# Kernel optimization log

Measured on AMD Instinct MI355X. Metric: run time of the kernel, lower is better.

The kernel has to match this reference:

```python
import jax, jax.numpy as jnp
import numpy as np

V = 32000   # vocab_size
S = 4096    # seq_len
D = 1024    # dim
H = 4096    # hidden_dim
L = 2       # num_layers
CS = 64     # chunk_size
R = 256     # low_rank_dim = max(8, D//4)
WIN = 8     # window_size (OptitationLayer default)
NEG = -1e30


def setup_inputs() -> dict:
    key = jax.random.key(0)
    ks = jax.random.split(key, 20)
    f32 = jnp.float32
    inp = {}
    inp['idx_seq'] = jax.random.randint(ks[0], (S,), 0, V)
    inp['embeddings'] = jax.random.normal(ks[1], (V, D), f32) * 0.01
    inp['positional'] = jax.random.normal(ks[2], (S, D), f32) * 0.01
    # per-layer MLP params, stacked over layer axis
    inp['Wg'] = jax.random.normal(ks[3], (L, D, D), f32) / D ** 0.5
    inp['bg'] = jnp.zeros((L, D), f32)
    inp['Ws'] = jax.random.normal(ks[4], (L, D, H), f32) / D ** 0.5
    inp['bs'] = jnp.zeros((L, H), f32)
    inp['Wo'] = jax.random.normal(ks[5], (L, H, D), f32) / H ** 0.5
    inp['bo'] = jnp.zeros((L, D), f32)
    # per-layer optitation (windowed attention) params
    inp['Wq'] = jax.random.normal(ks[6], (L, D, R), f32) / D ** 0.5
    inp['Wk'] = jax.random.normal(ks[7], (L, D, R), f32) / D ** 0.5
    inp['Wv'] = jax.random.normal(ks[8], (L, D, R), f32) / D ** 0.5
    inp['Wao'] = jax.random.normal(ks[9], (L, R, D), f32) / R ** 0.5
    inp['bq'] = jnp.zeros((L, R), f32)
    inp['bk'] = jnp.zeros((L, R), f32)
    inp['bv'] = jnp.zeros((L, R), f32)
    inp['bao'] = jnp.zeros((L, D), f32)
    inp['outW'] = jax.random.normal(ks[10], (D, V), f32) / D ** 0.5
    inp['outb'] = jnp.zeros((V,), f32)
    return inp


def _optitation(x, Wq, bq, Wk, bk, Wv, bv, Wao, bao):
    Q = x @ Wq + bq
    K = x @ Wk + bk
    Vv = x @ Wv + bv
    s = x.shape[0]
    off = jnp.arange(WIN + 1)
    j = jnp.arange(s)[:, None] - off[None, :]  # [s, w+1] key indices
    valid = j >= 0
    jc = jnp.maximum(j, 0)
    Kw = K[jc]   # [s, w+1, R]
    Vw = Vv[jc]  # [s, w+1, R]
    scores = jnp.einsum('sr,swr->sw', Q, Kw) / jnp.sqrt(jnp.float32(R))
    scores = jnp.where(valid, scores, NEG)
    attn = jax.nn.softmax(scores, axis=-1)
    ao = jnp.einsum('sw,swr->sr', attn, Vw)   # [s, R]
    return ao @ Wao + bao


def _chunk_link(x):
    # chunk-averaging with half-weighted neighbor chunks
    s, d = x.shape
    pad = (-s) % CS
    xp = jnp.pad(x, ((0, pad), (0, 0)))
    n = xp.shape[0] // CS
    c = xp.reshape(n, CS, d)
    prev = jnp.concatenate([jnp.zeros_like(c[:1]), c[:-1]], axis=0)
    nxt = jnp.concatenate([c[1:], jnp.zeros_like(c[:1])], axis=0)
    i = jnp.arange(n)
    w = 1.0 + 0.5 * (i > 0).astype(x.dtype) + 0.5 * (i < n - 1).astype(x.dtype)
    upd = (c + 0.5 * prev + 0.5 * nxt) / w[:, None, None]
    return upd.reshape(-1, d)[:s]


def reference(idx_seq, embeddings, positional, Wg, bg, Ws, bs, Wo, bo,
              Wq, bq, Wk, bk, Wv, bv, Wao, bao, outW, outb):
    s = idx_seq.shape[0]
    x = embeddings[idx_seq] + positional[:s]
    # decay accumulation: x[pos] += 0.8**pos * x[0] for pos >= 1 (x[0] untouched)
    decay = jnp.power(jnp.float32(0.8), jnp.arange(s, dtype=jnp.float32))
    decay = decay.at[0].set(0.0)
    x = x + decay[:, None] * x[0]
    for l in range(L):
        residual = x
        x = x * jax.nn.sigmoid(x @ Wg[l] + bg[l])            # lensed gate
        x = jnp.tanh(x @ Ws[l] + bs[l]) @ Wo[l] + bo[l]       # context sculpt
        x = x + residual
        x = x + _optitation(x, Wq[l], bq[l], Wk[l], bk[l],
                            Wv[l], bv[l], Wao[l], bao[l])
        x = _chunk_link(x)
    return x @ outW + outb
```

## Files before the change

kernel.cpp:

```cpp
#include <hip/hip_runtime.h>
#include <hip/hip_bf16.h>
#include <math.h>

#define S_LEN 4096
#define DIM   1024
#define HID   4096
#define NLAYER 2
#define RDIM  256
#define VOCAB 32000
#define QKVN  768

typedef unsigned short u16;
typedef __attribute__((ext_vector_type(8))) short s16x8;
typedef __attribute__((ext_vector_type(4))) float f32x4;
typedef __attribute__((ext_vector_type(4))) unsigned short u16x4;

__device__ inline u16 f2b(float f){
  unsigned u = __float_as_uint(f);
  u += 0x7fff + ((u >> 16) & 1);
  return (u16)(u >> 16);
}

__device__ inline void gload_lds16(const void* g, void* l){
  __builtin_amdgcn_global_load_lds((__attribute__((address_space(1))) void*)(g),
                                   (__attribute__((address_space(3))) void*)(l), 16, 0, 0);
}

__global__ void k_prep(const float* __restrict__ Wg,  const float* __restrict__ Ws,
                       const float* __restrict__ Wo,  const float* __restrict__ Wq,
                       const float* __restrict__ Wk,  const float* __restrict__ Wv,
                       const float* __restrict__ Wao, const float* __restrict__ outW,
                       u16* __restrict__ WgT, u16* __restrict__ WsT, u16* __restrict__ WoT,
                       u16* __restrict__ WqkvT, u16* __restrict__ WaoT, u16* __restrict__ outWT,
                       const float* __restrict__ bq, const float* __restrict__ bk,
                       const float* __restrict__ bv, float* __restrict__ bqkv2,
                       const int* __restrict__ idx, const float* __restrict__ emb,
                       const float* __restrict__ pos, float* __restrict__ xf,
                       u16* __restrict__ xb){
  __shared__ float tile[64][65];
  int tx = threadIdx.x, ty = threadIdx.y;
  int t = ty * 16 + tx;
  int id = blockIdx.x;
  if (id < 16384){
    int s = id >> 2;
    int d = (id & 3) * 256 + t;
    float v = emb[(size_t)idx[s] * DIM + d] + pos[(size_t)s * DIM + d];
    if (s > 0){
      float x0 = emb[(size_t)idx[0] * DIM + d] + pos[d];
      v += exp2f((float)s * -0.3219280948873623f) * x0;
    }
    size_t o = (size_t)s * DIM + d;
    xf[o] = v; xb[o] = f2b(v);
    return;
  }
  id -= 16384;
  if (id < 6){
    int l = id / 3, sel = id % 3;
    const float* s = sel == 0 ? bq : (sel == 1 ? bk : bv);
    bqkv2[l * 768 + sel * 256 + t] = s[(size_t)l * 256 + t];
    return;
  }
  id -= 6;
  const float* src; u16* dst; int K, N, bx, by;
  if (id < 512){
    int z = id >> 8, lo = id & 255;
    src = Wg + (size_t)z * DIM * DIM; dst = WgT + (size_t)z * DIM * DIM;
    K = DIM; N = DIM; bx = lo & 15; by = lo >> 4;
  } else if (id < 2560){
    int local = id - 512; int z = local >> 10, lo = local & 1023;
    src = Ws + (size_t)z * DIM * HID; dst = WsT + (size_t)z * DIM * HID;
    K = DIM; N = HID; bx = lo & 63; by = lo >> 6;
  } else if (id < 4608){
    int local = id - 2560; int z = local >> 10, lo = local & 1023;
    src = Wo + (size_t)z * HID * DIM; dst = WoT + (size_t)z * HID * DIM;
    K = HID; N = DIM; bx = lo & 15; by = lo >> 4;
  } else if (id < 4736){
    int local = id - 4608; int z = local >> 6, lo = local & 63;
    src = Wq + (size_t)z * DIM * RDIM; dst = WqkvT + (size_t)z * QKVN * DIM;
    K = DIM; N = RDIM; bx = lo & 3; by = lo >> 2;
  } else if (id < 4864){
    int local = id - 4736; int z = local >> 6, lo = local & 63;
    src = Wk + (size_t)z * DIM * RDIM; dst = WqkvT + (size_t)z * QKVN * DIM + (size_t)256 * DIM;
    K = DIM; N = RDIM; bx = lo & 3; by = lo >> 2;
  } else if (id < 4992){
    int local = id - 4864; int z = local >> 6, lo = local & 63;
    src = Wv + (size_t)z * DIM * RDIM; dst = WqkvT + (size_t)z * QKVN * DIM + (size_t)512 * DIM;
    K = DIM; N = RDIM; bx = lo & 3; by = lo >> 2;
  } else if (id < 5120){
    int local = id - 4992; int z = local >> 6, lo = local & 63;
    src = Wao + (size_t)z * RDIM * DIM; dst = WaoT + (size_t)z * RDIM * DIM;
    K = RDIM; N = DIM; bx = lo & 15; by = lo >> 4;
  } else {
    int local = id - 5120;
    src = outW; dst = outWT;
    K = DIM; N = VOCAB; bx = local % 500; by = local / 500;
  }
  int n0 = bx * 64, k0 = by * 64;
  #pragma unroll
  for (int i = 0; i < 4; i++){
    float4 v = *(const float4*)&src[(size_t)(k0 + ty + 16 * i) * N + n0 + tx * 4];
    tile[ty + 16 * i][tx * 4 + 0] = v.x;
    tile[ty + 16 * i][tx * 4 + 1] = v.y;
    tile[ty + 16 * i][tx * 4 + 2] = v.z;
    tile[ty + 16 * i][tx * 4 + 3] = v.w;
  }
  __syncthreads();
  #pragma unroll
  for (int i = 0; i < 4; i++){
    u16x4 o;
    #pragma unroll
    for (int j = 0; j < 4; j++) o[j] = f2b(tile[tx * 4 + j][ty + 16 * i]);
    *(u16x4*)&dst[(size_t)(n0 + ty + 16 * i) * K + k0 + tx * 4] = o;
  }
}

#define EP_GATE  0
#define EP_TANH  1
#define EP_RESID 2
#define EP_BIASF 3
#define EP_AO    4
#define EP_OUT   5

#define PH_SYNC() do{ asm volatile("" ::: "memory"); __builtin_amdgcn_s_barrier(); asm volatile("" ::: "memory"); }while(0)


#define MMA_QUAD(MH, NLO, BF) \
  { _Pragma("unroll") for (int mi = 0; mi < 4; mi++){ \
    _Pragma("unroll") for (int ni = 0; ni < 2; ni++){ \
      _Pragma("unroll") for (int ks = 0; ks < 2; ks++){ \
        acc[(MH)*4+mi][(NLO)+ni] = __builtin_amdgcn_mfma_f32_16x16x32_bf16((BF)[ni*2+ks], af[mi*2+ks], acc[(MH)*4+mi][(NLO)+ni], 0, 0, 0); } } } }

#define LDA(MH, BO) \
  { _Pragma("unroll") for (int mi = 0; mi < 4; mi++){ \
    _Pragma("unroll") for (int ks = 0; ks < 2; ks++){ \
      af[mi*2+ks] = *(const s16x8*)(pa0 + (BO) + ((MH)*4+mi)*1024 + ((ks ^ kb) * 32)); } } }

#define LDB(NH, BO) \
  { _Pragma("unroll") for (int ni = 0; ni < 2; ni++){ \
    _Pragma("unroll") for (int ks = 0; ks < 2; ks++){ \
      bf_[(NH)*4+ni*2+ks] = *(const s16x8*)(pb0 + (BO) + ((NH)*2+ni)*1024 + ((ks ^ kb) * 32)); } } }

__global__ __launch_bounds__(512, 2) void k_gemmL(
    const u16* __restrict__ A, const u16* __restrict__ Bt,
    const float* __restrict__ bias, float* __restrict__ outf,
    int N, int K, int tilesM, int tilesN){
  extern __shared__ u16 lds[];
  const int t = threadIdx.x;
  const int w = t >> 6, l = t & 63;
  const int wr = w >> 2, wc = w & 3;
  const int NT = K >> 6;
  const int NI = NT >> 1;
  const int nTiles = tilesM * tilesN;

  const int r0 = t >> 3;
  const int scol = (((t & 7) ^ ((t >> 3) & 7)) * 8);
  const int cb = (((l >> 4) ^ (l & 3)) * 8);
  const int kb = (l >> 2) & 1;
  const u16* pa0 = lds + (wr * 128 + (l & 15)) * 64 + cb;
  const u16* pb0 = lds + 32768 + (wc * 64 + (l & 15)) * 64 + cb;

  auto decode = [&](int idx2, int& bR, int& bC){
    int pr = tilesN * 2;
    int stripe = idx2 / pr, r2 = idx2 % pr;
    bR = (stripe * 2 + (r2 & 1)) * 256;
    bC = (r2 >> 1) * 256;
  };

  int tileIdx = blockIdx.x;
  if (tileIdx >= nTiles) return;
  int bRow, bCol, nRow = 0, nCol = 0;
  bool hasNext = false;
  decode(tileIdx, bRow, bCol);

  auto stage_half = [&](int tau, int q){
    const u16* base;
    if (tau >= NT){
      if (!hasNext) return;
      tau -= NT;
      base = (q < 2) ? A + (size_t)nRow * K : Bt + (size_t)nCol * K;
    } else {
      base = (q < 2) ? A + (size_t)bRow * K : Bt + (size_t)bCol * K;
    }
    int h = q & 1;
    const u16* gp = base + (size_t)(h * 128 + r0) * K + (size_t)tau * 64 + scol;
    u16* d = lds + ((q < 2) ? 0 : 32768) + ((tau & 1) * 16384) + h * 8192 + t * 8;
    gload_lds16(gp, d);
    gload_lds16(gp + (size_t)64 * K, d + 4096);
  };

  f32x4 acc[8][4] = {};
  s16x8 af[8], bf_[8];

  stage_half(0, 0); stage_half(0, 1); stage_half(0, 2); stage_half(0, 3);
  stage_half(1, 0);
  asm volatile("s_waitcnt vmcnt(2)" ::: "memory");
  PH_SYNC();

  for (; tileIdx < nTiles; tileIdx += gridDim.x){
    int nIdx = tileIdx + gridDim.x;
    hasNext = nIdx < nTiles;
    if (hasNext) decode(nIdx, nRow, nCol);

    for (int i = 0; i < NI; i++){
      const int t1 = 2 * i + 1, t2 = 2 * i + 2, t3 = 2 * i + 3;
      const bool lastGate = (!hasNext) && (i + 1 == NI);
      LDA(0, 0); LDB(0, 0);
      stage_half(t1, 1);
      PH_SYNC();
      __builtin_amdgcn_s_setprio(1); MMA_QUAD(0, 0, bf_); __builtin_amdgcn_s_setprio(0);
      PH_SYNC();
      LDB(1, 0);
      stage_half(t1, 2);
      PH_SYNC();
      __builtin_amdgcn_s_setprio(1); MMA_QUAD(0, 2, bf_ + 4); __builtin_amdgcn_s_setprio(0);
      PH_SYNC();
      LDA(1, 0);
      stage_half(t1, 3);
      PH_SYNC();
      __builtin_amdgcn_s_setprio(1); MMA_QUAD(1, 2, bf_ + 4); __builtin_amdgcn_s_setprio(0);
      PH_SYNC();
      stage_half(t2, 0);
      if (!lastGate) asm volatile("s_waitcnt vmcnt(2)" ::: "memory");
      else           asm volatile("s_waitcnt vmcnt(0)" ::: "memory");
      PH_SYNC();
      __builtin_amdgcn_s_setprio(1); MMA_QUAD(1, 0, bf_); __builtin_amdgcn_s_setprio(0);
      PH_SYNC();
      LDA(0, 16384); LDB(0, 16384);
      stage_half(t2, 1);
      PH_SYNC();
      __builtin_amdgcn_s_setprio(1); MMA_QUAD(0, 0, bf_); __builtin_amdgcn_s_setprio(0);
      PH_SYNC();
      LDB(1, 16384);
      stage_half(t2, 2);
      PH_SYNC();
      __builtin_amdgcn_s_setprio(1); MMA_QUAD(0, 2, bf_ + 4); __builtin_amdgcn_s_setprio(0);
      PH_SYNC();
      LDA(1, 16384);
      stage_half(t2, 3);
      PH_SYNC();
      __builtin_amdgcn_s_setprio(1); MMA_QUAD(1, 2, bf_ + 4); __builtin_amdgcn_s_setprio(0);
      PH_SYNC();
      stage_half(t3, 0);
      if (!lastGate) asm volatile("s_waitcnt vmcnt(2)" ::: "memory");
      PH_SYNC();
      __builtin_amdgcn_s_setprio(1); MMA_QUAD(1, 0, bf_); __builtin_amdgcn_s_setprio(0);
      PH_SYNC();
    }

    #pragma unroll
    for (int m = 0; m < 8; m++){
      int gr = bRow + wr * 128 + m * 16 + (l & 15);
      #pragma unroll
      for (int n = 0; n < 4; n++){
        int gc = bCol + wc * 64 + n * 16 + ((l >> 4) * 4);
        f32x4 v = acc[m][n] + *(const f32x4*)(bias + gc);
        *(f32x4*)(outf + (size_t)gr * N + gc) = v;
        acc[m][n] = (f32x4){0.f, 0.f, 0.f, 0.f};
      }
    }
    bRow = nRow; bCol = nCol;
  }
}

#define MMA2(MH, NL) \
  { _Pragma("unroll") for (int mi = 0; mi < 2; mi++){ \
    _Pragma("unroll") for (int ks = 0; ks < 2; ks++){ \
      acc[(MH)*2+mi][(NL)] = __builtin_amdgcn_mfma_f32_16x16x32_bf16(bf_[(NL)*2+ks], af[mi*2+ks], acc[(MH)*2+mi][(NL)], 0, 0, 0); } } }

#define LDA2(MH, BO) \
  { _Pragma("unroll") for (int mi = 0; mi < 2; mi++){ \
    _Pragma("unroll") for (int ks = 0; ks < 2; ks++){ \
      af[mi*2+ks] = *(const s16x8*)(pa0 + (BO) + ((MH)*2+mi)*1024 + ((ks ^ kb) * 32)); } } }

#define LDB2(NL, BO) \
  { _Pragma("unroll") for (int ks = 0; ks < 2; ks++){ \
    bf_[(NL)*2+ks] = *(const s16x8*)(pb0 + (BO) + (NL)*1024 + ((ks ^ kb) * 32)); } }

template<int EPI>
__global__ __launch_bounds__(512, 4) void k_gemm8b(
    const u16* __restrict__ A, const u16* __restrict__ Bt,
    const float* __restrict__ bias, const float* __restrict__ aux,
    float* __restrict__ outf, u16* __restrict__ outbf,
    int N, int K, int tilesM, int tilesN){
  extern __shared__ u16 lds[];
  const int t = threadIdx.x;
  const int w = t >> 6, l = t & 63;
  const int wr = w >> 2, wc = w & 3;
  const int NT = K >> 6;
  const int NI = NT >> 1;

  int nwg = tilesM * tilesN;
  int id = blockIdx.x, id2;
  if ((nwg & 7) == 0){ int c = nwg >> 3; id2 = (id & 7) * c + (id >> 3); }
  else id2 = id;
  int per = tilesM << 3;
  int g = id2 / per, r = id2 % per;
  int bm = r % tilesM;
  int bn = (g << 3) + r / tilesM;
  const int bRow = bm * 128, bCol = bn * 128;

  const int r0 = t >> 3;
  const int scol = (((t & 7) ^ ((t >> 3) & 7)) * 8);

  auto stage_half = [&](int tau, int q){
    if (tau >= NT) return;
    int h = q & 1;
    bool isA = q < 2;
    const u16* gp = (isA ? A + (size_t)bRow * K : Bt + (size_t)bCol * K)
                 + (size_t)(h * 64 + r0) * K + (size_t)tau * 64 + scol;
    u16* d = lds + (isA ? 0 : 16384) + ((tau & 1) * 8192) + h * 4096 + t * 8;
    gload_lds16(gp, d);
  };

  const int cb = (((l >> 4) ^ (l & 3)) * 8);
  const int kb = (l >> 2) & 1;
  const u16* pa0 = lds + wr * 4096 + (l & 15) * 64 + cb;
  const u16* pb0 = lds + 16384 + (wc >> 1) * 4096 + ((wc & 1) * 32 + (l & 15)) * 64 + cb;

  f32x4 acc[4][2] = {};
  s16x8 af[4], bf_[4];

  stage_half(0, 0); stage_half(0, 1); stage_half(0, 2); stage_half(0, 3);
  stage_half(1, 0);
  asm volatile("s_waitcnt vmcnt(1)" ::: "memory");
  PH_SYNC();

  for (int i = 0; i < NI; i++){
    const int t1 = 2 * i + 1, t2 = 2 * i + 2, t3 = 2 * i + 3;
    const bool last = (i + 1 == NI);
    LDA2(0, 0); LDB2(0, 0);
    stage_half(t1, 1);
    PH_SYNC();
    __builtin_amdgcn_s_setprio(1); MMA2(0, 0); __builtin_amdgcn_s_setprio(0);
    PH_SYNC();
    LDB2(1, 0);
    stage_half(t1, 2);
    PH_SYNC();
    __builtin_amdgcn_s_setprio(1); MMA2(0, 1); __builtin_amdgcn_s_setprio(0);
    PH_SYNC();
    LDA2(1, 0);
    stage_half(t1, 3);
    PH_SYNC();
    __builtin_amdgcn_s_setprio(1); MMA2(1, 1); __builtin_amdgcn_s_setprio(0);
    PH_SYNC();
    stage_half(t2, 0);
    if (!last) asm volatile("s_waitcnt vmcnt(1)" ::: "memory");
    else       asm volatile("s_waitcnt vmcnt(0)" ::: "memory");
    PH_SYNC();
    __builtin_amdgcn_s_setprio(1); MMA2(1, 0); __builtin_amdgcn_s_setprio(0);
    PH_SYNC();
    LDA2(0, 8192); LDB2(0, 8192);
    stage_half(t2, 1);
    PH_SYNC();
    __builtin_amdgcn_s_setprio(1); MMA2(0, 0); __builtin_amdgcn_s_setprio(0);
    PH_SYNC();
    LDB2(1, 8192);
    stage_half(t2, 2);
    PH_SYNC();
    __builtin_amdgcn_s_setprio(1); MMA2(0, 1); __builtin_amdgcn_s_setprio(0);
    PH_SYNC();
    LDA2(1, 8192);
    stage_half(t2, 3);
    PH_SYNC();
    __builtin_amdgcn_s_setprio(1); MMA2(1, 1); __builtin_amdgcn_s_setprio(0);
    PH_SYNC();
    stage_half(t3, 0);
    if (!last) asm volatile("s_waitcnt vmcnt(1)" ::: "memory");
    PH_SYNC();
    __builtin_amdgcn_s_setprio(1); MMA2(1, 0); __builtin_amdgcn_s_setprio(0);
    PH_SYNC();
  }

  #pragma unroll
  for (int m = 0; m < 4; m++){
    int gr = bRow + wr * 64 + m * 16 + (l & 15);
    #pragma unroll
    for (int n = 0; n < 2; n++){
      int gc = bCol + wc * 32 + n * 16 + ((l >> 4) * 4);
      size_t o = (size_t)gr * N + gc;
      f32x4 v = acc[m][n] + *(const f32x4*)(bias + gc);
      if constexpr (EPI == EP_GATE){
        f32x4 a = *(const f32x4*)(aux + o);
        u16x4 rr;
        #pragma unroll
        for (int q = 0; q < 4; q++) rr[q] = f2b(a[q] / (1.f + expf(-v[q])));
        *(u16x4*)(outbf + o) = rr;
      } else if constexpr (EPI == EP_TANH){
        u16x4 rr;
        #pragma unroll
        for (int q = 0; q < 4; q++) rr[q] = f2b(tanhf(v[q]));
        *(u16x4*)(outbf + o) = rr;
      } else if constexpr (EPI == EP_RESID){
        v += *(const f32x4*)(aux + o);
        *(f32x4*)(outf + o) = v;
        u16x4 rr;
        #pragma unroll
        for (int q = 0; q < 4; q++) rr[q] = f2b(v[q]);
        *(u16x4*)(outbf + o) = rr;
      } else if constexpr (EPI == EP_BIASF){
        *(f32x4*)(outf + o) = v;
      } else if constexpr (EPI == EP_AO){
        v += *(const f32x4*)(aux + o);
        *(f32x4*)(outf + o) = v;
      } else {
        *(f32x4*)(outf + o) = v;
      }
    }
  }
}

__global__ void k_attn(const float* __restrict__ qkv, u16* __restrict__ aob){
  int s = blockIdx.x * 4 + (threadIdx.x >> 6);
  int l = threadIdx.x & 63;
  const float* qp = qkv + (size_t)s * QKVN;
  float qr[4];
  #pragma unroll
  for (int r = 0; r < 4; r++) qr[r] = qp[l + 64 * r];
  float sc[9];
  float mx = -1e30f;
  #pragma unroll
  for (int j = 0; j <= 8; j++){
    int sj = s - j;
    bool ok = sj >= 0;
    int row = ok ? sj : 0;
    const float* kp = qkv + (size_t)row * QKVN + RDIM;
    float p = 0.f;
    #pragma unroll
    for (int r = 0; r < 4; r++) p += qr[r] * kp[l + 64 * r];
    #pragma unroll
    for (int off = 32; off; off >>= 1) p += __shfl_xor(p, off);
    p = ok ? p * 0.0625f : -1e30f;
    sc[j] = p;
    mx = fmaxf(mx, p);
  }
  float den = 0.f;
  #pragma unroll
  for (int j = 0; j <= 8; j++){ sc[j] = expf(sc[j] - mx); den += sc[j]; }
  float inv = 1.f / den;
  #pragma unroll
  for (int r = 0; r < 4; r++){
    float a = 0.f;
    #pragma unroll
    for (int j = 0; j <= 8; j++){
      int sj = s - j;
      int row = sj >= 0 ? sj : 0;
      a += sc[j] * qkv[(size_t)row * QKVN + 512 + l + 64 * r];
    }
    aob[(size_t)s * RDIM + l + 64 * r] = f2b(a * inv);
  }
}

__global__ void k_chunk(const float* __restrict__ xin, float* __restrict__ xout,
                        u16* __restrict__ xb){
  int s = blockIdx.x;
  int d = blockIdx.y * 256 + threadIdx.x;
  int ci = s >> 6;
  float v = xin[(size_t)s * DIM + d];
  float wsum = 1.f;
  if (ci > 0){ v += 0.5f * xin[(size_t)(s - 64) * DIM + d]; wsum += 0.5f; }
  if (ci < 63){ v += 0.5f * xin[(size_t)(s + 64) * DIM + d]; wsum += 0.5f; }
  v /= wsum;
  size_t o = (size_t)s * DIM + d;
  xout[o] = v; xb[o] = f2b(v);
}

extern "C" void kernel_launch(void* const* d_in, const int* in_sizes, int n_in,
                              void* d_out, int out_size, void* d_ws, size_t ws_size,
                              hipStream_t stream){
  const int*   idx  = (const int*)d_in[0];
  const float* emb  = (const float*)d_in[1];
  const float* pos  = (const float*)d_in[2];
  const float* Wg   = (const float*)d_in[3];
  const float* bg   = (const float*)d_in[4];
  const float* Ws_  = (const float*)d_in[5];
  const float* bs   = (const float*)d_in[6];
  const float* Wo   = (const float*)d_in[7];
  const float* bo   = (const float*)d_in[8];
  const float* Wq   = (const float*)d_in[9];
  const float* Wk   = (const float*)d_in[10];
  const float* Wv   = (const float*)d_in[11];
  const float* Wao  = (const float*)d_in[12];
  const float* bq   = (const float*)d_in[13];
  const float* bk   = (const float*)d_in[14];
  const float* bv   = (const float*)d_in[15];
  const float* bao  = (const float*)d_in[16];
  const float* outW = (const float*)d_in[17];
  const float* outb = (const float*)d_in[18];
  float* out = (float*)d_out;

  char* p = (char*)d_ws;
  auto alloc = [&](size_t n)->char*{ char* r = p; p += (n + 255) & ~(size_t)255; return r; };
  float* xfA  = (float*)alloc((size_t)S_LEN * DIM * 4);
  float* xfB  = (float*)alloc((size_t)S_LEN * DIM * 4);
  u16*   xb   = (u16*)  alloc((size_t)S_LEN * DIM * 2);
  u16*   xgb  = (u16*)  alloc((size_t)S_LEN * DIM * 2);
  u16*   tbuf = (u16*)  alloc((size_t)S_LEN * HID * 2);
  float* qkvf = (float*)alloc((size_t)S_LEN * QKVN * 4);
  u16*   aob  = (u16*)  alloc((size_t)S_LEN * RDIM * 2);
  float* bqkv2= (float*)alloc(2 * QKVN * 4);
  u16*   WgT  = (u16*)  alloc((size_t)NLAYER * DIM * DIM * 2);
  u16*   WsT  = (u16*)  alloc((size_t)NLAYER * DIM * HID * 2);
  u16*   WoT  = (u16*)  alloc((size_t)NLAYER * HID * DIM * 2);
  u16*   WqkvT= (u16*)  alloc((size_t)NLAYER * QKVN * DIM * 2);
  u16*   WaoT = (u16*)  alloc((size_t)NLAYER * RDIM * DIM * 2);
  u16*   outWT= (u16*)  alloc((size_t)VOCAB * DIM * 2);

  (void)hipFuncSetAttribute((const void*)&k_gemmL,
                      hipFuncAttributeMaxDynamicSharedMemorySize, 131072);
  (void)hipFuncSetAttribute((const void*)&k_gemm8b<EP_GATE>,
                      hipFuncAttributeMaxDynamicSharedMemorySize, 65536);
  (void)hipFuncSetAttribute((const void*)&k_gemm8b<EP_TANH>,
                      hipFuncAttributeMaxDynamicSharedMemorySize, 65536);
  (void)hipFuncSetAttribute((const void*)&k_gemm8b<EP_RESID>,
                      hipFuncAttributeMaxDynamicSharedMemorySize, 65536);
  (void)hipFuncSetAttribute((const void*)&k_gemm8b<EP_BIASF>,
                      hipFuncAttributeMaxDynamicSharedMemorySize, 65536);
  (void)hipFuncSetAttribute((const void*)&k_gemm8b<EP_AO>,
                      hipFuncAttributeMaxDynamicSharedMemorySize, 65536);

  k_prep<<<29510, dim3(16, 16), 0, stream>>>(Wg, Ws_, Wo, Wq, Wk, Wv, Wao, outW,
                                             WgT, WsT, WoT, WqkvT, WaoT, outWT,
                                             bq, bk, bv, bqkv2,
                                             idx, emb, pos, xfA, xb);

  float* curF = xfA; float* altF = xfB;
  for (int l = 0; l < NLAYER; l++){
    k_gemm8b<EP_GATE ><<<(S_LEN/128)*(DIM/128),  512, 65536, stream>>>(xb,  WgT  + (size_t)l*DIM*DIM,  bg + (size_t)l*DIM, curF, nullptr, xgb, DIM, DIM, S_LEN/128, DIM/128);
    k_gemm8b<EP_TANH ><<<(S_LEN/128)*(HID/128),  512, 65536, stream>>>(xgb, WsT  + (size_t)l*DIM*HID,  bs + (size_t)l*HID, nullptr, nullptr, tbuf, HID, DIM, S_LEN/128, HID/128);
    k_gemm8b<EP_RESID><<<(S_LEN/128)*(DIM/128),  512, 65536, stream>>>(tbuf,WoT  + (size_t)l*HID*DIM,  bo + (size_t)l*DIM, curF, curF, xb, DIM, HID, S_LEN/128, DIM/128);
    k_gemm8b<EP_BIASF><<<(S_LEN/128)*(QKVN/128), 512, 65536, stream>>>(xb,  WqkvT + (size_t)l*QKVN*DIM, bqkv2 + (size_t)l*QKVN, nullptr, qkvf, nullptr, QKVN, DIM, S_LEN/128, QKVN/128);
    k_attn<<<S_LEN/4, 256, 0, stream>>>(qkvf, aob);
    k_gemm8b<EP_AO   ><<<(S_LEN/128)*(DIM/128),  512, 65536, stream>>>(aob, WaoT + (size_t)l*RDIM*DIM, bao + (size_t)l*DIM, curF, curF, nullptr, DIM, RDIM, S_LEN/128, DIM/128);
    k_chunk<<<dim3(S_LEN, DIM/256), 256, 0, stream>>>(curF, altF, xb);
    float* tmp = curF; curF = altF; altF = tmp;
  }
  k_gemmL<<<256, 512, 131072, stream>>>(xb, outWT, outb, out, VOCAB, DIM, S_LEN/256, VOCAB/256);
}
```

Before: 822.6 us.

## Add 64x128-tile GEMM kernel for narrow-N layers to raise workgroup count

Adds a new k_gemm4 kernel that uses 64x128 output tiles instead of 128x128, with a double-buffered LDS pipeline and launch bounds allowing more resident workgroups. It is used for the gate, output-projection, QKV and attention-output GEMMs, whose N is 1024 or 768, so these launches get twice as many workgroups to fill the GPU's compute units. The large hidden-dimension tanh GEMM keeps the old kernel. Smaller tiles mean less operand reuse per loaded byte and more total global traffic. The epilogue is also factored into a shared helper.

```diff
diff --git a/kernel.cpp b/kernel.cpp
--- a/kernel.cpp
+++ b/kernel.cpp
@@ -123,6 +123,36 @@
 
 #define PH_SYNC() do{ asm volatile("" ::: "memory"); __builtin_amdgcn_s_barrier(); asm volatile("" ::: "memory"); }while(0)
 
+template<int EPI>
+__device__ inline void epi_store(f32x4 v, size_t o, const float* aux,
+                                 float* outf, u16* outbf){
+  if constexpr (EPI == EP_GATE){
+    f32x4 a = *(const f32x4*)(aux + o);
+    u16x4 rr;
+    #pragma unroll
+    for (int q = 0; q < 4; q++) rr[q] = f2b(a[q] / (1.f + expf(-v[q])));
+    *(u16x4*)(outbf + o) = rr;
+  } else if constexpr (EPI == EP_TANH){
+    u16x4 rr;
+    #pragma unroll
+    for (int q = 0; q < 4; q++) rr[q] = f2b(tanhf(v[q]));
+    *(u16x4*)(outbf + o) = rr;
+  } else if constexpr (EPI == EP_RESID){
+    v += *(const f32x4*)(aux + o);
+    *(f32x4*)(outf + o) = v;
+    u16x4 rr;
+    #pragma unroll
+    for (int q = 0; q < 4; q++) rr[q] = f2b(v[q]);
+    *(u16x4*)(outbf + o) = rr;
+  } else if constexpr (EPI == EP_BIASF){
+    *(f32x4*)(outf + o) = v;
+  } else if constexpr (EPI == EP_AO){
+    v += *(const f32x4*)(aux + o);
+    *(f32x4*)(outf + o) = v;
+  } else {
+    *(f32x4*)(outf + o) = v;
+  }
+}
 
 #define MMA_QUAD(MH, NLO, BF) \
   { _Pragma("unroll") for (int mi = 0; mi < 4; mi++){ \
@@ -377,34 +407,113 @@
     #pragma unroll
     for (int n = 0; n < 2; n++){
       int gc = bCol + wc * 32 + n * 16 + ((l >> 4) * 4);
-      size_t o = (size_t)gr * N + gc;
       f32x4 v = acc[m][n] + *(const f32x4*)(bias + gc);
-      if constexpr (EPI == EP_GATE){
-        f32x4 a = *(const f32x4*)(aux + o);
-        u16x4 rr;
-        #pragma unroll
-        for (int q = 0; q < 4; q++) rr[q] = f2b(a[q] / (1.f + expf(-v[q])));
-        *(u16x4*)(outbf + o) = rr;
-      } else if constexpr (EPI == EP_TANH){
-        u16x4 rr;
-        #pragma unroll
-        for (int q = 0; q < 4; q++) rr[q] = f2b(tanhf(v[q]));
-        *(u16x4*)(outbf + o) = rr;
-      } else if constexpr (EPI == EP_RESID){
-        v += *(const f32x4*)(aux + o);
-        *(f32x4*)(outf + o) = v;
-        u16x4 rr;
-        #pragma unroll
-        for (int q = 0; q < 4; q++) rr[q] = f2b(v[q]);
-        *(u16x4*)(outbf + o) = rr;
-      } else if constexpr (EPI == EP_BIASF){
-        *(f32x4*)(outf + o) = v;
-      } else if constexpr (EPI == EP_AO){
-        v += *(const f32x4*)(aux + o);
-        *(f32x4*)(outf + o) = v;
-      } else {
-        *(f32x4*)(outf + o) = v;
-      }
+      epi_store<EPI>(v, (size_t)gr * N + gc, aux, outf, outbf);
+    }
+  }
+}
+
+
+#define MMA4(NL) \
+  { _Pragma("unroll") for (int mi = 0; mi < 2; mi++){ \
+    _Pragma("unroll") for (int ks = 0; ks < 2; ks++){ \
+      acc[mi][(NL)] = __builtin_amdgcn_mfma_f32_16x16x32_bf16(bf_[(NL)*2+ks], af[mi*2+ks], acc[mi][(NL)], 0, 0, 0); } } }
+
+#define LDA4(BO) \
+  { _Pragma("unroll") for (int mi = 0; mi < 2; mi++){ \
+    _Pragma("unroll") for (int ks = 0; ks < 2; ks++){ \
+      af[mi*2+ks] = *(const s16x8*)(pa0 + (BO) + mi*1024 + ((ks ^ kb) * 32)); } } }
+
+#define LDB4(NL, BO) \
+  { _Pragma("unroll") for (int ks = 0; ks < 2; ks++){ \
+    bf_[(NL)*2+ks] = *(const s16x8*)(pb0 + (BO) + (NL)*1024 + ((ks ^ kb) * 32)); } }
+
+template<int EPI>
+__global__ __launch_bounds__(512, 6) void k_gemm4(
+    const u16* __restrict__ A, const u16* __restrict__ Bt,
+    const float* __restrict__ bias, const float* __restrict__ aux,
+    float* __restrict__ outf, u16* __restrict__ outbf,
+    int N, int K, int tilesM, int tilesN){
+  extern __shared__ u16 lds[];
+  const int t = threadIdx.x;
+  const int w = t >> 6, l = t & 63;
+  const int wr = w >> 2, wc = w & 3;
+  const int NT = K >> 6;
+  const int NI = NT >> 1;
+
+  int nwg = tilesM * tilesN;
+  int id = blockIdx.x, id2;
+  if ((nwg & 7) == 0){ int c = nwg >> 3; id2 = (id & 7) * c + (id >> 3); }
+  else id2 = id;
+  int per = tilesM << 3;
+  int g = id2 / per, r = id2 % per;
+  int bm = r % tilesM;
+  int bn = (g << 3) + r / tilesM;
+  const int bRow = bm * 64, bCol = bn * 128;
+
+  const int r0 = t >> 3;
+  const int scol = (((t & 7) ^ ((t >> 3) & 7)) * 8);
+
+  auto stage = [&](int tau, int q){
+    if (tau >= NT) return;
+    bool isA = q == 0;
+    int h = q & 1;
+    const u16* gp = (isA ? A + (size_t)(bRow + r0) * K
+                         : Bt + (size_t)(bCol + h * 64 + r0) * K)
+                  + (size_t)tau * 64 + scol;
+    u16* d = lds + (isA ? (tau & 1) * 4096
+                        : 8192 + (tau & 1) * 8192 + h * 4096) + t * 8;
+    gload_lds16(gp, d);
+  };
+
+  const int cb = (((l >> 4) ^ (l & 3)) * 8);
+  const int kb = (l >> 2) & 1;
+  const u16* pa0 = lds + (wr * 32 + (l & 15)) * 64 + cb;
+  const u16* pb0 = lds + 8192 + (wc >> 1) * 4096 + ((wc & 1) * 32 + (l & 15)) * 64 + cb;
+
+  f32x4 acc[2][2] = {};
+  s16x8 af[4], bf_[4];
+
+  stage(0, 0); stage(0, 2); stage(0, 3);
+  asm volatile("s_waitcnt vmcnt(0)" ::: "memory");
+  PH_SYNC();
+
+  for (int i = 0; i < NI; i++){
+    const int t1 = 2 * i + 1, t2 = 2 * i + 2, t3 = 2 * i + 3;
+    const bool last = (i + 1 == NI);
+    LDA4(0); LDB4(0, 0);
+    stage(t1, 0);
+    PH_SYNC();
+    __builtin_amdgcn_s_setprio(1); MMA4(0); __builtin_amdgcn_s_setprio(0);
+    PH_SYNC();
+    LDB4(1, 0);
+    stage(t1, 2); stage(t1, 3); stage(t2, 0);
+    if (!last) asm volatile("s_waitcnt vmcnt(1)" ::: "memory");
+    else       asm volatile("s_waitcnt vmcnt(0)" ::: "memory");
+    PH_SYNC();
+    __builtin_amdgcn_s_setprio(1); MMA4(1); __builtin_amdgcn_s_setprio(0);
+    PH_SYNC();
+    LDA4(4096); LDB4(0, 8192);
+    stage(t2, 2);
+    PH_SYNC();
+    __builtin_amdgcn_s_setprio(1); MMA4(0); __builtin_amdgcn_s_setprio(0);
+    PH_SYNC();
+    LDB4(1, 8192);
+    stage(t2, 3); stage(t3, 0);
+    if (!last) asm volatile("s_waitcnt vmcnt(1)" ::: "memory");
+    PH_SYNC();
+    __builtin_amdgcn_s_setprio(1); MMA4(1); __builtin_amdgcn_s_setprio(0);
+    PH_SYNC();
+  }
+
+  #pragma unroll
+  for (int m = 0; m < 2; m++){
+    int gr = bRow + wr * 32 + m * 16 + (l & 15);
+    #pragma unroll
+    for (int n = 0; n < 2; n++){
+      int gc = bCol + wc * 32 + n * 16 + ((l >> 4) * 4);
+      f32x4 v = acc[m][n] + *(const f32x4*)(bias + gc);
+      epi_store<EPI>(v, (size_t)gr * N + gc, aux, outf, outbf);
     }
   }
 }
@@ -507,16 +616,16 @@
 
   (void)hipFuncSetAttribute((const void*)&k_gemmL,
                       hipFuncAttributeMaxDynamicSharedMemorySize, 131072);
-  (void)hipFuncSetAttribute((const void*)&k_gemm8b<EP_GATE>,
-                      hipFuncAttributeMaxDynamicSharedMemorySize, 65536);
   (void)hipFuncSetAttribute((const void*)&k_gemm8b<EP_TANH>,
                       hipFuncAttributeMaxDynamicSharedMemorySize, 65536);
-  (void)hipFuncSetAttribute((const void*)&k_gemm8b<EP_RESID>,
-                      hipFuncAttributeMaxDynamicSharedMemorySize, 65536);
-  (void)hipFuncSetAttribute((const void*)&k_gemm8b<EP_BIASF>,
-                      hipFuncAttributeMaxDynamicSharedMemorySize, 65536);
-  (void)hipFuncSetAttribute((const void*)&k_gemm8b<EP_AO>,
-                      hipFuncAttributeMaxDynamicSharedMemorySize, 65536);
+  (void)hipFuncSetAttribute((const void*)&k_gemm4<EP_GATE>,
+                      hipFuncAttributeMaxDynamicSharedMemorySize, 49152);
+  (void)hipFuncSetAttribute((const void*)&k_gemm4<EP_RESID>,
+                      hipFuncAttributeMaxDynamicSharedMemorySize, 49152);
+  (void)hipFuncSetAttribute((const void*)&k_gemm4<EP_BIASF>,
+                      hipFuncAttributeMaxDynamicSharedMemorySize, 49152);
+  (void)hipFuncSetAttribute((const void*)&k_gemm4<EP_AO>,
+                      hipFuncAttributeMaxDynamicSharedMemorySize, 49152);
 
   k_prep<<<29510, dim3(16, 16), 0, stream>>>(Wg, Ws_, Wo, Wq, Wk, Wv, Wao, outW,
                                              WgT, WsT, WoT, WqkvT, WaoT, outWT,
@@ -525,12 +634,12 @@
 
   float* curF = xfA; float* altF = xfB;
   for (int l = 0; l < NLAYER; l++){
-    k_gemm8b<EP_GATE ><<<(S_LEN/128)*(DIM/128),  512, 65536, stream>>>(xb,  WgT  + (size_t)l*DIM*DIM,  bg + (size_t)l*DIM, curF, nullptr, xgb, DIM, DIM, S_LEN/128, DIM/128);
-    k_gemm8b<EP_TANH ><<<(S_LEN/128)*(HID/128),  512, 65536, stream>>>(xgb, WsT  + (size_t)l*DIM*HID,  bs + (size_t)l*HID, nullptr, nullptr, tbuf, HID, DIM, S_LEN/128, HID/128);
-    k_gemm8b<EP_RESID><<<(S_LEN/128)*(DIM/128),  512, 65536, stream>>>(tbuf,WoT  + (size_t)l*HID*DIM,  bo + (size_t)l*DIM, curF, curF, xb, DIM, HID, S_LEN/128, DIM/128);
-    k_gemm8b<EP_BIASF><<<(S_LEN/128)*(QKVN/128), 512, 65536, stream>>>(xb,  WqkvT + (size_t)l*QKVN*DIM, bqkv2 + (size_t)l*QKVN, nullptr, qkvf, nullptr, QKVN, DIM, S_LEN/128, QKVN/128);
+    k_gemm4<EP_GATE ><<<(S_LEN/64)*(DIM/128),  512, 49152, stream>>>(xb,  WgT  + (size_t)l*DIM*DIM,  bg + (size_t)l*DIM, curF, nullptr, xgb, DIM, DIM, S_LEN/64, DIM/128);
+    k_gemm8b<EP_TANH><<<(S_LEN/128)*(HID/128), 512, 65536, stream>>>(xgb, WsT  + (size_t)l*DIM*HID,  bs + (size_t)l*HID, nullptr, nullptr, tbuf, HID, DIM, S_LEN/128, HID/128);
+    k_gemm4<EP_RESID><<<(S_LEN/64)*(DIM/128),  512, 49152, stream>>>(tbuf,WoT  + (size_t)l*HID*DIM,  bo + (size_t)l*DIM, curF, curF, xb, DIM, HID, S_LEN/64, DIM/128);
+    k_gemm4<EP_BIASF><<<(S_LEN/64)*(QKVN/128), 512, 49152, stream>>>(xb,  WqkvT + (size_t)l*QKVN*DIM, bqkv2 + (size_t)l*QKVN, nullptr, qkvf, nullptr, QKVN, DIM, S_LEN/64, QKVN/128);
     k_attn<<<S_LEN/4, 256, 0, stream>>>(qkvf, aob);
-    k_gemm8b<EP_AO   ><<<(S_LEN/128)*(DIM/128),  512, 65536, stream>>>(aob, WaoT + (size_t)l*RDIM*DIM, bao + (size_t)l*DIM, curF, curF, nullptr, DIM, RDIM, S_LEN/128, DIM/128);
+    k_gemm4<EP_AO   ><<<(S_LEN/64)*(DIM/128),  512, 49152, stream>>>(aob, WaoT + (size_t)l*RDIM*DIM, bao + (size_t)l*DIM, curF, curF, nullptr, DIM, RDIM, S_LEN/64, DIM/128);
     k_chunk<<<dim3(S_LEN, DIM/256), 256, 0, stream>>>(curF, altF, xb);
     float* tmp = curF; curF = altF; altF = tmp;
   }
```

Result: faster. 799.4 us (-2.8%).
